# Optimization experiments

Measured on AMD Instinct MI355X. Metric: run time of the kernel, lower is better.

## Reference

```python
import jax, jax.numpy as jnp
import numpy as np

REFRACTORY_PERIOD = 5
DAMPENING_FACTOR = 0.3


def setup_inputs() -> dict:
    key = jax.random.key(0)
    B, T, N = 32, 4096, 256
    x = jax.random.normal(key, (B, T, N), dtype=jnp.float32)
    return {"x": x}


def _refractory_scan(x):
    # x: [B, T, N]; scan over time keeping refractory counter q resident.
    B, T, N = x.shape
    xt = jnp.swapaxes(x, 0, 1)  # [T, B, N]

    def step(q, x_t):
        cond = (x_t > 0) & (q == 0)
        z_t = jnp.where(cond, jnp.ones_like(q), jnp.zeros_like(q))
        q = jnp.maximum(jnp.zeros_like(q), q - 1) + REFRACTORY_PERIOD * z_t
        return q, z_t

    q0 = jnp.zeros((B, N), dtype=x.dtype)
    # Note: the t=0 case in the original (z0 = x0>0, q = R*z0) is exactly the
    # first step of this scan starting from q0 = 0.
    _, z = jax.lax.scan(step, q0, xt)
    return jnp.swapaxes(z, 0, 1)  # [B, T, N]


def reference(x) -> jnp.ndarray:
    # Forward value is exactly z_forward (the surrogate-gradient straight-through
    # construction leaves the value unchanged).
    return _refractory_scan(x)
```

## Files before the change

### kernel.cpp

```cpp
#include <hip/hip_runtime.h>
#include <cstdint>
#include <cstddef>

#define BB 32
#define TT 4096
#define NN 256
#define CC 128
#define PP (TT / CC)


__global__ __launch_bounds__(256) void pass1_exits(const float* __restrict__ x,
                                                   uint32_t* __restrict__ exits) {
    const int n = threadIdx.x;
    const int p = blockIdx.x;
    const int b = blockIdx.y;
    const float* xp = x + ((size_t)b * TT + (size_t)p * CC) * NN + n;

    int na0 = 0, na1 = 1, na2 = 2, na3 = 3, na4 = 4, na5 = 5;
    #pragma unroll 8
    for (int j = 0; j < CC; ++j) {
        const bool pos = xp[(size_t)j * NN] > 0.0f;
        const int nj = j + 6;
        if (pos & (j >= na0)) na0 = nj;
        if (pos & (j >= na1)) na1 = nj;
        if (pos & (j >= na2)) na2 = nj;
        if (pos & (j >= na3)) na3 = nj;
        if (pos & (j >= na4)) na4 = nj;
        if (pos & (j >= na5)) na5 = nj;
    }
    const uint32_t q0 = (uint32_t)(na0 > CC ? na0 - CC : 0);
    const uint32_t q1 = (uint32_t)(na1 > CC ? na1 - CC : 0);
    const uint32_t q2 = (uint32_t)(na2 > CC ? na2 - CC : 0);
    const uint32_t q3 = (uint32_t)(na3 > CC ? na3 - CC : 0);
    const uint32_t q4 = (uint32_t)(na4 > CC ? na4 - CC : 0);
    const uint32_t q5 = (uint32_t)(na5 > CC ? na5 - CC : 0);
    const uint32_t packed = q0 | (q1 << 4) | (q2 << 8) | (q3 << 12) |
                            (q4 << 16) | (q5 << 20);
    exits[((size_t)b * PP + p) * NN + n] = packed;
}

__global__ __launch_bounds__(256) void pass2_scan(const uint32_t* __restrict__ exits,
                                                  uint8_t* __restrict__ entry) {
    const int n = threadIdx.x;
    const int b = blockIdx.x;
    int q = 0;
    #pragma unroll
    for (int p = 0; p < PP; ++p) {
        const size_t idx = ((size_t)b * PP + p) * NN + n;
        entry[idx] = (uint8_t)q;
        const uint32_t e = exits[idx];
        q = (int)((e >> (4 * q)) & 0xFu);
    }
}

__global__ __launch_bounds__(256) void pass3_emit(const float* __restrict__ x,
                                                  const uint8_t* __restrict__ entry,
                                                  float* __restrict__ z) {
    const int n = threadIdx.x;
    const int p = blockIdx.x;
    const int b = blockIdx.y;
    const size_t base = ((size_t)b * TT + (size_t)p * CC) * NN + n;
    int na = (int)entry[((size_t)b * PP + p) * NN + n];
    #pragma unroll 8
    for (int j = 0; j < CC; ++j) {
        const bool pos = x[base + (size_t)j * NN] > 0.0f;
        const bool sp = pos & (j >= na);
        z[base + (size_t)j * NN] = sp ? 1.0f : 0.0f;
        if (sp) na = j + 6;
    }
}

extern "C" void kernel_launch(void* const* d_in, const int* in_sizes, int n_in,
                              void* d_out, int out_size, void* d_ws, size_t ws_size,
                              hipStream_t stream) {
    const float* x = (const float*)d_in[0];
    float* z = (float*)d_out;

    uint32_t* exits = (uint32_t*)d_ws;
    uint8_t* entry = (uint8_t*)((char*)d_ws + (size_t)BB * PP * NN * sizeof(uint32_t));

    dim3 grid1(PP, BB);
    pass1_exits<<<grid1, 256, 0, stream>>>(x, exits);
    pass2_scan<<<BB, 256, 0, stream>>>(exits, entry);
    pass3_emit<<<grid1, 256, 0, stream>>>(x, entry, z);
}
```

Before: 254.6 us.

## Fuse three-pass refractory scan into single kernel with decoupled look-back chaining

Replaces the three launches (chunk exit tables, serial chunk scan, emit) with one fused kernel. Each thread handles four neurons via float4 loads and keeps the positive-sign bits in registers, so x is read once instead of twice. Blocks covering consecutive time groups pass their exit state forward through spin-waited flags in workspace, which is reset by a memset each call. The cost is a serial dependency chain across 8 block groups per batch, fewer blocks (256), and heavier register use, and progress relies on earlier blocks being scheduled before later ones.

```diff
diff --git a/kernel.cpp b/kernel.cpp
--- a/kernel.cpp
+++ b/kernel.cpp
@@ -4,69 +4,128 @@
 
 #define BB 32
 #define TT 4096
-#define NN 256
+#define NNV 64
 #define CC 128
-#define PP (TT / CC)
+#define PSUB 4
+#define PG 8
+#define MSG_WORDS 32
 
+__global__ __launch_bounds__(256) void refrac_fused(const float* __restrict__ x,
+                                                    float* __restrict__ z,
+                                                    uint32_t* __restrict__ msg) {
+    const int tid = threadIdx.x;
+    const int pg = blockIdx.x >> 5;
+    const int b  = blockIdx.x & 31;
+    const int psub = tid >> 6;
+    const int n4 = tid & 63;
+    const int p = pg * PSUB + psub;
 
-__global__ __launch_bounds__(256) void pass1_exits(const float* __restrict__ x,
-                                                   uint32_t* __restrict__ exits) {
-    const int n = threadIdx.x;
-    const int p = blockIdx.x;
-    const int b = blockIdx.y;
-    const float* xp = x + ((size_t)b * TT + (size_t)p * CC) * NN + n;
+    const float4* __restrict__ xv = reinterpret_cast<const float4*>(x)
+        + ((size_t)b * TT + (size_t)p * CC) * NNV + n4;
 
-    int na0 = 0, na1 = 1, na2 = 2, na3 = 3, na4 = 4, na5 = 5;
-    #pragma unroll 8
-    for (int j = 0; j < CC; ++j) {
-        const bool pos = xp[(size_t)j * NN] > 0.0f;
-        const int nj = j + 6;
-        if (pos & (j >= na0)) na0 = nj;
-        if (pos & (j >= na1)) na1 = nj;
-        if (pos & (j >= na2)) na2 = nj;
-        if (pos & (j >= na3)) na3 = nj;
-        if (pos & (j >= na4)) na4 = nj;
-        if (pos & (j >= na5)) na5 = nj;
+    int na[4][6];
+    #pragma unroll
+    for (int c = 0; c < 4; ++c)
+        #pragma unroll
+        for (int e = 0; e < 6; ++e) na[c][e] = e;
+
+    uint32_t bits[4][4];
+
+    #pragma unroll
+    for (int w = 0; w < 4; ++w) {
+        uint32_t cur[4] = {0u, 0u, 0u, 0u};
+        for (int jb = 0; jb < 32; jb += 8) {
+            float4 buf[8];
+            #pragma unroll
+            for (int u = 0; u < 8; ++u)
+                buf[u] = xv[(size_t)(w * 32 + jb + u) * NNV];
+            #pragma unroll
+            for (int u = 0; u < 8; ++u) {
+                const int j2 = jb + u;
+                const int j  = w * 32 + j2;
+                const float4 v = buf[u];
+                const float fv[4] = {v.x, v.y, v.z, v.w};
+                #pragma unroll
+                for (int c = 0; c < 4; ++c) {
+                    const bool pos = fv[c] > 0.0f;
+                    cur[c] |= pos ? (1u << j2) : 0u;
+                    #pragma unroll
+                    for (int e = 0; e < 6; ++e)
+                        if (pos & (j >= na[c][e])) na[c][e] = j + 6;
+                }
+            }
+        }
+        #pragma unroll
+        for (int c = 0; c < 4; ++c) bits[c][w] = cur[c];
     }
-    const uint32_t q0 = (uint32_t)(na0 > CC ? na0 - CC : 0);
-    const uint32_t q1 = (uint32_t)(na1 > CC ? na1 - CC : 0);
-    const uint32_t q2 = (uint32_t)(na2 > CC ? na2 - CC : 0);
-    const uint32_t q3 = (uint32_t)(na3 > CC ? na3 - CC : 0);
-    const uint32_t q4 = (uint32_t)(na4 > CC ? na4 - CC : 0);
-    const uint32_t q5 = (uint32_t)(na5 > CC ? na5 - CC : 0);
-    const uint32_t packed = q0 | (q1 << 4) | (q2 << 8) | (q3 << 12) |
-                            (q4 << 16) | (q5 << 20);
-    exits[((size_t)b * PP + p) * NN + n] = packed;
-}
 
-__global__ __launch_bounds__(256) void pass2_scan(const uint32_t* __restrict__ exits,
-                                                  uint8_t* __restrict__ entry) {
-    const int n = threadIdx.x;
-    const int b = blockIdx.x;
-    int q = 0;
+    __shared__ uint32_t tbl_lds[PSUB][256];
+    __shared__ uint8_t  ent_lds[PSUB][256];
+    __shared__ uint8_t  sout_lds[256];
+
     #pragma unroll
-    for (int p = 0; p < PP; ++p) {
-        const size_t idx = ((size_t)b * PP + p) * NN + n;
-        entry[idx] = (uint8_t)q;
-        const uint32_t e = exits[idx];
-        q = (int)((e >> (4 * q)) & 0xFu);
+    for (int c = 0; c < 4; ++c) {
+        uint32_t tbl = 0;
+        #pragma unroll
+        for (int e = 0; e < 6; ++e) {
+            int q = na[c][e] - CC;
+            q = q > 0 ? q : 0;
+            tbl |= (uint32_t)q << (4 * e);
+        }
+        tbl_lds[psub][n4 * 4 + c] = tbl;
     }
-}
+    __syncthreads();
 
-__global__ __launch_bounds__(256) void pass3_emit(const float* __restrict__ x,
-                                                  const uint8_t* __restrict__ entry,
-                                                  float* __restrict__ z) {
-    const int n = threadIdx.x;
-    const int p = blockIdx.x;
-    const int b = blockIdx.y;
-    const size_t base = ((size_t)b * TT + (size_t)p * CC) * NN + n;
-    int na = (int)entry[((size_t)b * PP + p) * NN + n];
-    #pragma unroll 8
-    for (int j = 0; j < CC; ++j) {
-        const bool pos = x[base + (size_t)j * NN] > 0.0f;
-        const bool sp = pos & (j >= na);
-        z[base + (size_t)j * NN] = sp ? 1.0f : 0.0f;
-        if (sp) na = j + 6;
+    {
+        const int n = tid;
+        int e = 0;
+        if (pg > 0) {
+            const uint32_t* inw = msg + ((size_t)b * PG + (pg - 1)) * MSG_WORDS + (n >> 3);
+            uint32_t wv;
+            while ((wv = __hip_atomic_load(inw, __ATOMIC_RELAXED,
+                                           __HIP_MEMORY_SCOPE_AGENT)) & 0x88888888u)
+                __builtin_amdgcn_s_sleep(1);
+            e = (int)((wv >> ((n & 7) * 4)) & 0xFu);
+        }
+        #pragma unroll
+        for (int s = 0; s < PSUB; ++s) {
+            ent_lds[s][n] = (uint8_t)e;
+            e = (int)((tbl_lds[s][n] >> (4 * e)) & 0xFu);
+        }
+        sout_lds[n] = (uint8_t)e;
+    }
+    __syncthreads();
+
+    if (pg < PG - 1 && tid < MSG_WORDS) {
+        uint32_t wv = 0;
+        #pragma unroll
+        for (int k = 0; k < 8; ++k)
+            wv |= (uint32_t)sout_lds[tid * 8 + k] << (4 * k);
+        __hip_atomic_store(msg + ((size_t)b * PG + pg) * MSG_WORDS + tid, wv,
+                           __ATOMIC_RELAXED, __HIP_MEMORY_SCOPE_AGENT);
+    }
+
+    float4* __restrict__ zv = reinterpret_cast<float4*>(z)
+        + ((size_t)b * TT + (size_t)p * CC) * NNV + n4;
+
+    int ea[4];
+    #pragma unroll
+    for (int c = 0; c < 4; ++c) ea[c] = (int)ent_lds[psub][n4 * 4 + c];
+
+    #pragma unroll
+    for (int w = 0; w < 4; ++w) {
+        const uint32_t bw[4] = {bits[0][w], bits[1][w], bits[2][w], bits[3][w]};
+        for (int j2 = 0; j2 < 32; ++j2) {
+            const int j = w * 32 + j2;
+            float o[4];
+            #pragma unroll
+            for (int c = 0; c < 4; ++c) {
+                const bool sp = (((bw[c] >> j2) & 1u) != 0u) & (j >= ea[c]);
+                if (sp) ea[c] = j + 6;
+                o[c] = sp ? 1.0f : 0.0f;
+            }
+            zv[(size_t)j * NNV] = make_float4(o[0], o[1], o[2], o[3]);
+        }
     }
 }
 
@@ -75,12 +134,9 @@
                               hipStream_t stream) {
     const float* x = (const float*)d_in[0];
     float* z = (float*)d_out;
+    uint32_t* msg = (uint32_t*)d_ws;
 
-    uint32_t* exits = (uint32_t*)d_ws;
-    uint8_t* entry = (uint8_t*)((char*)d_ws + (size_t)BB * PP * NN * sizeof(uint32_t));
+    hipMemsetAsync(d_ws, 0xAA, (size_t)BB * PG * MSG_WORDS * sizeof(uint32_t), stream);
 
-    dim3 grid1(PP, BB);
-    pass1_exits<<<grid1, 256, 0, stream>>>(x, exits);
-    pass2_scan<<<BB, 256, 0, stream>>>(exits, entry);
-    pass3_emit<<<grid1, 256, 0, stream>>>(x, entry, z);
+    refrac_fused<<<dim3(BB * PG), 256, 0, stream>>>(x, z, msg);
 }
```

Result: faster. 245.7 us (-3.5%).
